# Optimization experiments

Hardware: AMD Instinct MI355X
Metric: run time of the kernel (lower is better)

The kernel has to match this reference:

```python
import jax, jax.numpy as jnp
import numpy as np

N, E, IN_F, H_F, OUT_F = 50000, 800000, 128, 128, 3
BN_EPS = 1e-5


def setup_inputs() -> dict:
    key = jax.random.key(0)
    ks = jax.random.split(key, 8)
    x = jax.random.normal(ks[0], (N, IN_F), dtype=jnp.float32)
    edge_index = jax.random.randint(ks[1], (2, E), 0, N, dtype=jnp.int64)
    edge_weight = jax.random.uniform(ks[2], (E,), dtype=jnp.float32)
    # GCNConv weight (Glorot-style scale) and bias
    conv_w = jax.random.normal(ks[3], (IN_F, H_F), dtype=jnp.float32) * (1.0 / np.sqrt(IN_F))
    conv_b = jnp.zeros((H_F,), dtype=jnp.float32)
    # BatchNorm affine params
    gamma = jnp.ones((H_F,), dtype=jnp.float32)
    beta = jnp.zeros((H_F,), dtype=jnp.float32)
    # Final linear
    lin_w = jax.random.normal(ks[4], (H_F, OUT_F), dtype=jnp.float32) * (1.0 / np.sqrt(H_F))
    lin_b = jnp.zeros((OUT_F,), dtype=jnp.float32)
    return {"x": x, "edge_index": edge_index, "edge_weight": edge_weight,
            "conv_w": conv_w, "conv_b": conv_b, "gamma": gamma, "beta": beta,
            "lin_w": lin_w, "lin_b": lin_b}


def _gcn_conv(x, edge_index, edge_weight, conv_w, conv_b):
    n = x.shape[0]
    # add self-loops with weight 1 (PyG GCNConv default)
    loops = jnp.arange(n, dtype=edge_index.dtype)
    row = jnp.concatenate([edge_index[0], loops])
    col = jnp.concatenate([edge_index[1], loops])
    ew = jnp.concatenate([edge_weight, jnp.ones((n,), dtype=edge_weight.dtype)])
    # symmetric normalization: deg over destination nodes
    deg = jax.ops.segment_sum(ew, col, num_segments=n)
    dinv = jnp.where(deg > 0, jax.lax.rsqrt(deg), 0.0)
    norm = dinv[row] * ew * dinv[col]            # [E+N]
    h = x @ conv_w                                # [N, h_f]
    msg = h[row] * norm[:, None]                  # gather + scale, [E+N, h_f]
    agg = jax.ops.segment_sum(msg, col, num_segments=n)  # scatter-add
    return agg + conv_b


def reference(x, edge_index, edge_weight, conv_w, conv_b, gamma, beta, lin_w, lin_b):
    h = jax.nn.relu(_gcn_conv(x, edge_index, edge_weight, conv_w, conv_b))
    # BatchNorm1d over the node dimension (training-style batch stats, biased var)
    mean = jnp.mean(h, axis=0)
    var = jnp.mean((h - mean) ** 2, axis=0)
    hn = (h - mean) * jax.lax.rsqrt(var + BN_EPS) * gamma + beta
    # dropout is identity (deterministic eval-style reference)
    return hn @ lin_w + lin_b
```

## Files before the change

kernel.cpp:

```cpp
#include <hip/hip_runtime.h>

#define NN   50000
#define NE   800000
#define FH   128
#define NOUT 3
#define BN_EPS 1e-5f

#define CAP  48
#define EWS  65535.0f
#define IEWS (1.0f / 65535.0f)
#define FXS  8388608.0f

#define GEMM_BLKS   782
#define BUCKET_BLKS 782
#define GATHER_BLKS 2048
#define RED_BLKS    (GATHER_BLKS / 256)

#define WS_H2      0
#define WS_AGG2    3200000
#define WS_BUCKET  6400000
#define WS_PACKED  8800000
#define WS_DINV    8900000
#define WS_PARTIAL 8950000
#define WS_STAGE2  9474288
#define WS_PREP    9476336

typedef __attribute__((ext_vector_type(8))) short  short8;
typedef __attribute__((ext_vector_type(4))) float  f32x4;

__device__ __forceinline__ unsigned int pack_bf16(float a, float b) {
    unsigned int ua = __float_as_uint(a);
    unsigned int ub = __float_as_uint(b);
    ua += 0x7fffu + ((ua >> 16) & 1u);
    ub += 0x7fffu + ((ub >> 16) & 1u);
    return (ua >> 16) | (ub & 0xffff0000u);
}
__device__ __forceinline__ unsigned short bf16_1(float a) {
    unsigned int ua = __float_as_uint(a);
    ua += 0x7fffu + ((ua >> 16) & 1u);
    return (unsigned short)(ua >> 16);
}
__device__ __forceinline__ float bf16_lo(unsigned int u) {
    return __uint_as_float(u << 16);
}
__device__ __forceinline__ float bf16_hi(unsigned int u) {
    return __uint_as_float(u & 0xffff0000u);
}

__global__ __launch_bounds__(256) void k_bucket(const int* __restrict__ ei,
                                                const float* __restrict__ ew,
                                                unsigned long long* __restrict__ packed,
                                                unsigned int* __restrict__ bucket) {
    const int e0 = blockIdx.x * 1024 + threadIdx.x;
    int                col[4];
    unsigned int       ent[4];
    unsigned long long add[4];
    int                ok[4];
#pragma unroll
    for (int k = 0; k < 4; ++k) {
        int e = e0 + k * 256;
        ok[k] = (e < NE);
        int ee = ok[k] ? e : 0;
        int row = ei[ee];
        col[k] = ei[NE + ee];
        float wv = ew[ee];
        ent[k] = ((unsigned int)row << 16) | __float2uint_rn(wv * EWS);
        add[k] = (1ULL << 32) | (unsigned long long)__float2uint_rn(wv * FXS);
    }
    int slot[4];
#pragma unroll
    for (int k = 0; k < 4; ++k)
        slot[k] = ok[k] ? (int)(atomicAdd(&packed[col[k]], add[k]) >> 32) : 0;
#pragma unroll
    for (int k = 0; k < 4; ++k)
        if (ok[k]) bucket[(size_t)col[k] * CAP + slot[k]] = ent[k];
}

__global__ __launch_bounds__(256) void k_gemm(const float* __restrict__ x,
                                              const float* __restrict__ w,
                                              unsigned int* __restrict__ h2,
                                              const unsigned long long* __restrict__ packed,
                                              float* __restrict__ dinv) {
    __shared__ unsigned short swB[32 * 64 * 8];
    const int tid = threadIdx.x;

    {
        int gi = blockIdx.x * 256 + tid;
        if (gi < NN) {
            unsigned int lo = (unsigned int)(packed[gi] & 0xffffffffu);
            dinv[gi] = rsqrtf((float)lo * (1.0f / FXS) + 1.0f);
        }
    }

#pragma unroll
    for (int it = 0; it < 8; ++it) {
        int s  = tid + it * 256;
        int l  = s & 63;
        int fs = s >> 6;
        int kc = fs >> 3, t = fs & 7;
        int n  = (l & 15) + 16 * t;
        int k0 = kc * 32 + (l >> 4) * 8;
        unsigned short* dst = &swB[s * 8];
#pragma unroll
        for (int j = 0; j < 8; ++j)
            dst[j] = bf16_1(w[(size_t)(k0 + j) * FH + n]);
    }
    __syncthreads();

    const int wv = tid >> 6, l = tid & 63;
    const int m = l & 15, q = l >> 4;
    int node = blockIdx.x * 64 + wv * 16 + m;
    if (node >= NN) node = NN - 1;

    f32x4 acc[8];
#pragma unroll
    for (int t = 0; t < 8; ++t) acc[t] = (f32x4){0.f, 0.f, 0.f, 0.f};

#pragma unroll
    for (int kc = 0; kc < 4; ++kc) {
        const float* xr = x + (size_t)node * FH + kc * 32 + q * 8;
        float4 a0 = *(const float4*)xr;
        float4 a1 = *(const float4*)(xr + 4);
        union { short8 s8; uint4 u4; } af;
        af.u4.x = pack_bf16(a0.x, a0.y);  af.u4.y = pack_bf16(a0.z, a0.w);
        af.u4.z = pack_bf16(a1.x, a1.y);  af.u4.w = pack_bf16(a1.z, a1.w);
#pragma unroll
        for (int t = 0; t < 8; ++t) {
            union { short8 s8; uint4 u4; } bf;
            bf.u4 = *(const uint4*)&swB[((kc * 8 + t) * 64 + l) * 8];
            acc[t] = __builtin_amdgcn_mfma_f32_16x16x32_bf16(af.s8, bf.s8, acc[t], 0, 0, 0);
        }
    }

    __syncthreads();
    unsigned short* sc = swB;
#pragma unroll
    for (int t = 0; t < 8; ++t) {
#pragma unroll
        for (int r = 0; r < 4; ++r) {
            int ml = wv * 16 + q * 4 + r;
            int f  = t * 16 + m;
            sc[ml * FH + f] = bf16_1(acc[t][r]);
        }
    }
    __syncthreads();
    const uint4* s4 = (const uint4*)sc;
#pragma unroll
    for (int i = 0; i < 4; ++i) {
        int u  = tid + i * 256;
        int nl = u >> 4;
        int ng = blockIdx.x * 64 + nl;
        if (ng < NN)
            *((uint4*)h2 + (size_t)ng * 16 + (u & 15)) = s4[u];
    }
}

__global__ __launch_bounds__(256) void k_gather(const unsigned int* __restrict__ h2,
                                                const float* __restrict__ dinv,
                                                const unsigned int* __restrict__ bucket,
                                                const unsigned long long* __restrict__ packed,
                                                const float* __restrict__ conv_b,
                                                unsigned int* __restrict__ agg2,
                                                float* __restrict__ partial) {
    const int lane = threadIdx.x & 63;
    const int wv   = threadIdx.x >> 6;
    float2 bv = *(const float2*)(conv_b + lane * 2);

    float sa = 0.f, sb = 0.f, sa2 = 0.f, sb2 = 0.f;

    for (int n = blockIdx.x * 4 + wv; n < NN; n += GATHER_BLKS * 4) {
        float dvn = dinv[n];
        unsigned int hself = h2[(size_t)n * 64 + lane];
        float ax = bf16_lo(hself) * dvn;
        float ay = bf16_hi(hself) * dvn;

        const unsigned int* bkt = bucket + (size_t)n * CAP;
        int c = (int)(packed[n] >> 32);
        int j = 0;
        for (; j + 8 <= c; j += 8) {
            uint4 b0 = *(const uint4*)(bkt + j);
            uint4 b1 = *(const uint4*)(bkt + j + 4);
            unsigned int u[8] = {b0.x, b0.y, b0.z, b0.w, b1.x, b1.y, b1.z, b1.w};
            float t[8];
            unsigned int q[8];
#pragma unroll
            for (int r = 0; r < 8; ++r) {
                int s = u[r] >> 16;
                t[r] = dinv[s] * (float)(u[r] & 0xffffu) * IEWS;
                q[r] = h2[(size_t)s * 64 + lane];
            }
#pragma unroll
            for (int r = 0; r < 8; ++r) {
                ax = fmaf(bf16_lo(q[r]), t[r], ax);
                ay = fmaf(bf16_hi(q[r]), t[r], ay);
            }
        }
        if (j + 4 <= c) {
            uint4 b0 = *(const uint4*)(bkt + j);
            unsigned int u[4] = {b0.x, b0.y, b0.z, b0.w};
#pragma unroll
            for (int r = 0; r < 4; ++r) {
                int s = u[r] >> 16;
                float t = dinv[s] * (float)(u[r] & 0xffffu) * IEWS;
                unsigned int q = h2[(size_t)s * 64 + lane];
                ax = fmaf(bf16_lo(q), t, ax);
                ay = fmaf(bf16_hi(q), t, ay);
            }
            j += 4;
        }
        for (; j < c; ++j) {
            unsigned int u0 = bkt[j];
            int s0 = u0 >> 16;
            float t0 = dinv[s0] * (float)(u0 & 0xffffu) * IEWS;
            unsigned int q0 = h2[(size_t)s0 * 64 + lane];
            ax = fmaf(bf16_lo(q0), t0, ax);  ay = fmaf(bf16_hi(q0), t0, ay);
        }

        float ox = fmaxf(fmaf(dvn, ax, bv.x), 0.f);
        float oy = fmaxf(fmaf(dvn, ay, bv.y), 0.f);
        agg2[(size_t)n * 64 + lane] = pack_bf16(ox, oy);

        sa += ox;  sa2 = fmaf(ox, ox, sa2);
        sb += oy;  sb2 = fmaf(oy, oy, sb2);
    }

    __shared__ float red[256];
    float vals[4] = {sa, sb, sa2, sb2};
    float* pb = partial + (size_t)blockIdx.x * 256;
#pragma unroll
    for (int r = 0; r < 4; ++r) {
        red[threadIdx.x] = vals[r];
        __syncthreads();
        if (wv == 0) {
            float t = red[lane] + red[lane + 64] + red[lane + 128] + red[lane + 192];
            pb[((r < 2) ? 0 : FH) + 2 * lane + (r & 1)] = t;
        }
        __syncthreads();
    }
}

__global__ __launch_bounds__(256) void k_red(const float* __restrict__ partial,
                                             float* __restrict__ stage2) {
    int i = threadIdx.x;
    const float* base = partial + (size_t)blockIdx.x * 256 * 256;
    float acc = 0.f;
    for (int j = 0; j < 256; ++j) acc += base[j * 256 + i];
    stage2[blockIdx.x * 256 + i] = acc;
}

__global__ void k_prep(const float* __restrict__ stage2,
                       const float* __restrict__ gamma,
                       const float* __restrict__ beta,
                       const float* __restrict__ lin_w,
                       const float* __restrict__ lin_b,
                       float* __restrict__ prep) {
    __shared__ float ssum[256];
    __shared__ float red[3 * FH];
    int i = threadIdx.x;
    float acc = 0.f;
#pragma unroll
    for (int r = 0; r < RED_BLKS; ++r) acc += stage2[r * 256 + i];
    ssum[i] = acc;
    __syncthreads();
    if (i < FH) {
        float mean = ssum[i] * (1.0f / NN);
        float var  = ssum[FH + i] * (1.0f / NN) - mean * mean;
        float inv  = rsqrtf(var + BN_EPS);
        float sc   = inv * gamma[i];
        float sh   = fmaf(-mean, sc, beta[i]);
#pragma unroll
        for (int o = 0; o < NOUT; ++o) {
            float lw = lin_w[i * NOUT + o];
            prep[i * NOUT + o] = sc * lw;
            red[o * FH + i]    = sh * lw;
        }
    }
    __syncthreads();
    if (i < NOUT) {
        float s = lin_b[i];
        for (int f = 0; f < FH; ++f) s += red[i * FH + f];
        prep[3 * FH + i] = s;
    }
}

__global__ __launch_bounds__(256) void k_final(const unsigned int* __restrict__ agg2,
                                               const float* __restrict__ prep,
                                               float* __restrict__ out) {
    int n = blockIdx.x * 4 + (threadIdx.x >> 6);
    int lane = threadIdx.x & 63;
    int f0 = lane * 2, f1 = lane * 2 + 1;

    unsigned int v = agg2[(size_t)n * 64 + lane];
    float vx = bf16_lo(v), vy = bf16_hi(v);

    float o0 = vx * prep[f0 * NOUT + 0] + vy * prep[f1 * NOUT + 0];
    float o1 = vx * prep[f0 * NOUT + 1] + vy * prep[f1 * NOUT + 1];
    float o2 = vx * prep[f0 * NOUT + 2] + vy * prep[f1 * NOUT + 2];

#pragma unroll
    for (int off = 32; off > 0; off >>= 1) {
        o0 += __shfl_down(o0, off, 64);
        o1 += __shfl_down(o1, off, 64);
        o2 += __shfl_down(o2, off, 64);
    }
    if (lane == 0) {
        out[n * NOUT + 0] = o0 + prep[3 * FH + 0];
        out[n * NOUT + 1] = o1 + prep[3 * FH + 1];
        out[n * NOUT + 2] = o2 + prep[3 * FH + 2];
    }
}

extern "C" void kernel_launch(void* const* d_in, const int* in_sizes, int n_in,
                              void* d_out, int out_size, void* d_ws, size_t ws_size,
                              hipStream_t stream) {
    const float* x      = (const float*)d_in[0];
    const int*   ei     = (const int*)d_in[1];
    const float* ew     = (const float*)d_in[2];
    const float* conv_w = (const float*)d_in[3];
    const float* conv_b = (const float*)d_in[4];
    const float* gamma  = (const float*)d_in[5];
    const float* beta   = (const float*)d_in[6];
    const float* lin_w  = (const float*)d_in[7];
    const float* lin_b  = (const float*)d_in[8];
    float* out = (float*)d_out;
    float* ws  = (float*)d_ws;

    unsigned int*       h2      = (unsigned int*)(ws + WS_H2);
    unsigned int*       agg2    = (unsigned int*)(ws + WS_AGG2);
    unsigned int*       bucket  = (unsigned int*)(ws + WS_BUCKET);
    unsigned long long* packed  = (unsigned long long*)(ws + WS_PACKED);
    float*              dinv    = ws + WS_DINV;
    float*              partial = ws + WS_PARTIAL;
    float*              stage2  = ws + WS_STAGE2;
    float*              prep    = ws + WS_PREP;

    hipMemsetAsync(packed, 0, (size_t)NN * sizeof(unsigned long long), stream);

    k_bucket<<<BUCKET_BLKS, 256, 0, stream>>>(ei, ew, packed, bucket);
    k_gemm  <<<GEMM_BLKS,   256, 0, stream>>>(x, conv_w, h2, packed, dinv);
    k_gather<<<GATHER_BLKS, 256, 0, stream>>>(h2, dinv, bucket, packed, conv_b, agg2, partial);
    k_red   <<<RED_BLKS,    256, 0, stream>>>(partial, stage2);
    k_prep  <<<1,           256, 0, stream>>>(stage2, gamma, beta, lin_w, lin_b, prep);
    k_final <<<NN / 4,      256, 0, stream>>>(agg2, prep, out);
}
```

Baseline: 194.6 us.

## Fuse edge bucketing with GEMM kernel and compute dinv on the fly in gather

Merges the edge-bucketing kernel and the feature GEMM into one launch, with even blocks doing the GEMM and odd blocks doing the bucketing, so the two independent phases run concurrently and one launch disappears. The dinv array is dropped. The gather kernel recomputes rsqrt of the degree for each neighbor from the low word of the packed counter, which removes a separate write and read pass. The cost is an extra rsqrt per edge and 8-byte-strided reads of the packed array in the gather.

```diff
diff --git a/kernel.cpp b/kernel.cpp
--- a/kernel.cpp
+++ b/kernel.cpp
@@ -10,9 +10,9 @@
 #define EWS  65535.0f
 #define IEWS (1.0f / 65535.0f)
 #define FXS  8388608.0f
-
-#define GEMM_BLKS   782
-#define BUCKET_BLKS 782
+#define IFXS (1.0f / 8388608.0f)
+
+#define FUSED_BLKS  1564
 #define GATHER_BLKS 2048
 #define RED_BLKS    (GATHER_BLKS / 256)
 
@@ -20,10 +20,9 @@
 #define WS_AGG2    3200000
 #define WS_BUCKET  6400000
 #define WS_PACKED  8800000
-#define WS_DINV    8900000
-#define WS_PARTIAL 8950000
-#define WS_STAGE2  9474288
-#define WS_PREP    9476336
+#define WS_PARTIAL 8900000
+#define WS_STAGE2  9424288
+#define WS_PREP    9426336
 
 typedef __attribute__((ext_vector_type(8))) short  short8;
 typedef __attribute__((ext_vector_type(4))) float  f32x4;
@@ -47,118 +46,110 @@
     return __uint_as_float(u & 0xffff0000u);
 }
 
-__global__ __launch_bounds__(256) void k_bucket(const int* __restrict__ ei,
-                                                const float* __restrict__ ew,
-                                                unsigned long long* __restrict__ packed,
-                                                unsigned int* __restrict__ bucket) {
-    const int e0 = blockIdx.x * 1024 + threadIdx.x;
-    int                col[4];
-    unsigned int       ent[4];
-    unsigned long long add[4];
-    int                ok[4];
-#pragma unroll
-    for (int k = 0; k < 4; ++k) {
-        int e = e0 + k * 256;
-        ok[k] = (e < NE);
-        int ee = ok[k] ? e : 0;
-        int row = ei[ee];
-        col[k] = ei[NE + ee];
-        float wv = ew[ee];
-        ent[k] = ((unsigned int)row << 16) | __float2uint_rn(wv * EWS);
-        add[k] = (1ULL << 32) | (unsigned long long)__float2uint_rn(wv * FXS);
-    }
-    int slot[4];
-#pragma unroll
-    for (int k = 0; k < 4; ++k)
-        slot[k] = ok[k] ? (int)(atomicAdd(&packed[col[k]], add[k]) >> 32) : 0;
-#pragma unroll
-    for (int k = 0; k < 4; ++k)
-        if (ok[k]) bucket[(size_t)col[k] * CAP + slot[k]] = ent[k];
-}
-
-__global__ __launch_bounds__(256) void k_gemm(const float* __restrict__ x,
-                                              const float* __restrict__ w,
-                                              unsigned int* __restrict__ h2,
-                                              const unsigned long long* __restrict__ packed,
-                                              float* __restrict__ dinv) {
+__global__ __launch_bounds__(256) void k_gemm_bucket(
+        const float* __restrict__ x, const float* __restrict__ w,
+        unsigned int* __restrict__ h2,
+        const int* __restrict__ ei, const float* __restrict__ ew,
+        unsigned long long* __restrict__ packed,
+        unsigned int* __restrict__ bucket) {
     __shared__ unsigned short swB[32 * 64 * 8];
     const int tid = threadIdx.x;
 
-    {
-        int gi = blockIdx.x * 256 + tid;
-        if (gi < NN) {
-            unsigned int lo = (unsigned int)(packed[gi] & 0xffffffffu);
-            dinv[gi] = rsqrtf((float)lo * (1.0f / FXS) + 1.0f);
-        }
-    }
-
-#pragma unroll
-    for (int it = 0; it < 8; ++it) {
-        int s  = tid + it * 256;
-        int l  = s & 63;
-        int fs = s >> 6;
-        int kc = fs >> 3, t = fs & 7;
-        int n  = (l & 15) + 16 * t;
-        int k0 = kc * 32 + (l >> 4) * 8;
-        unsigned short* dst = &swB[s * 8];
-#pragma unroll
-        for (int j = 0; j < 8; ++j)
-            dst[j] = bf16_1(w[(size_t)(k0 + j) * FH + n]);
-    }
-    __syncthreads();
-
-    const int wv = tid >> 6, l = tid & 63;
-    const int m = l & 15, q = l >> 4;
-    int node = blockIdx.x * 64 + wv * 16 + m;
-    if (node >= NN) node = NN - 1;
-
-    f32x4 acc[8];
-#pragma unroll
-    for (int t = 0; t < 8; ++t) acc[t] = (f32x4){0.f, 0.f, 0.f, 0.f};
-
-#pragma unroll
-    for (int kc = 0; kc < 4; ++kc) {
-        const float* xr = x + (size_t)node * FH + kc * 32 + q * 8;
-        float4 a0 = *(const float4*)xr;
-        float4 a1 = *(const float4*)(xr + 4);
-        union { short8 s8; uint4 u4; } af;
-        af.u4.x = pack_bf16(a0.x, a0.y);  af.u4.y = pack_bf16(a0.z, a0.w);
-        af.u4.z = pack_bf16(a1.x, a1.y);  af.u4.w = pack_bf16(a1.z, a1.w);
+    if ((blockIdx.x & 1) == 0) {
+        const int gblk = blockIdx.x >> 1;
+#pragma unroll
+        for (int it = 0; it < 8; ++it) {
+            int s  = tid + it * 256;
+            int l  = s & 63;
+            int fs = s >> 6;
+            int kc = fs >> 3, t = fs & 7;
+            int n  = (l & 15) + 16 * t;
+            int k0 = kc * 32 + (l >> 4) * 8;
+            unsigned short* dst = &swB[s * 8];
+#pragma unroll
+            for (int j = 0; j < 8; ++j)
+                dst[j] = bf16_1(w[(size_t)(k0 + j) * FH + n]);
+        }
+        __syncthreads();
+
+        const int wv = tid >> 6, l = tid & 63;
+        const int m = l & 15, q = l >> 4;
+        int node = gblk * 64 + wv * 16 + m;
+        if (node >= NN) node = NN - 1;
+
+        f32x4 acc[8];
+#pragma unroll
+        for (int t = 0; t < 8; ++t) acc[t] = (f32x4){0.f, 0.f, 0.f, 0.f};
+
+#pragma unroll
+        for (int kc = 0; kc < 4; ++kc) {
+            const float* xr = x + (size_t)node * FH + kc * 32 + q * 8;
+            float4 a0 = *(const float4*)xr;
+            float4 a1 = *(const float4*)(xr + 4);
+            union { short8 s8; uint4 u4; } af;
+            af.u4.x = pack_bf16(a0.x, a0.y);  af.u4.y = pack_bf16(a0.z, a0.w);
+            af.u4.z = pack_bf16(a1.x, a1.y);  af.u4.w = pack_bf16(a1.z, a1.w);
+#pragma unroll
+            for (int t = 0; t < 8; ++t) {
+                union { short8 s8; uint4 u4; } bf;
+                bf.u4 = *(const uint4*)&swB[((kc * 8 + t) * 64 + l) * 8];
+                acc[t] = __builtin_amdgcn_mfma_f32_16x16x32_bf16(af.s8, bf.s8, acc[t], 0, 0, 0);
+            }
+        }
+
+        __syncthreads();
+        unsigned short* sc = swB;
 #pragma unroll
         for (int t = 0; t < 8; ++t) {
-            union { short8 s8; uint4 u4; } bf;
-            bf.u4 = *(const uint4*)&swB[((kc * 8 + t) * 64 + l) * 8];
-            acc[t] = __builtin_amdgcn_mfma_f32_16x16x32_bf16(af.s8, bf.s8, acc[t], 0, 0, 0);
-        }
-    }
-
-    __syncthreads();
-    unsigned short* sc = swB;
-#pragma unroll
-    for (int t = 0; t < 8; ++t) {
-#pragma unroll
-        for (int r = 0; r < 4; ++r) {
-            int ml = wv * 16 + q * 4 + r;
-            int f  = t * 16 + m;
-            sc[ml * FH + f] = bf16_1(acc[t][r]);
-        }
-    }
-    __syncthreads();
-    const uint4* s4 = (const uint4*)sc;
-#pragma unroll
-    for (int i = 0; i < 4; ++i) {
-        int u  = tid + i * 256;
-        int nl = u >> 4;
-        int ng = blockIdx.x * 64 + nl;
-        if (ng < NN)
-            *((uint4*)h2 + (size_t)ng * 16 + (u & 15)) = s4[u];
+#pragma unroll
+            for (int r = 0; r < 4; ++r) {
+                int ml = wv * 16 + q * 4 + r;
+                int f  = t * 16 + m;
+                sc[ml * FH + f] = bf16_1(acc[t][r]);
+            }
+        }
+        __syncthreads();
+        const uint4* s4 = (const uint4*)sc;
+#pragma unroll
+        for (int i = 0; i < 4; ++i) {
+            int u  = tid + i * 256;
+            int nl = u >> 4;
+            int ng = gblk * 64 + nl;
+            if (ng < NN)
+                *((uint4*)h2 + (size_t)ng * 16 + (u & 15)) = s4[u];
+        }
+    } else {
+        const int bidx = blockIdx.x >> 1;
+        const int e0 = bidx * 1024 + tid;
+        int                col[4];
+        unsigned int       ent[4];
+        unsigned long long add[4];
+        int                ok[4];
+#pragma unroll
+        for (int k = 0; k < 4; ++k) {
+            int e = e0 + k * 256;
+            ok[k] = (e < NE);
+            int ee = ok[k] ? e : 0;
+            int row = ei[ee];
+            col[k] = ei[NE + ee];
+            float wv2 = ew[ee];
+            ent[k] = ((unsigned int)row << 16) | __float2uint_rn(wv2 * EWS);
+            add[k] = (1ULL << 32) | (unsigned long long)__float2uint_rn(wv2 * FXS);
+        }
+        int slot[4];
+#pragma unroll
+        for (int k = 0; k < 4; ++k)
+            slot[k] = ok[k] ? (int)(atomicAdd(&packed[col[k]], add[k]) >> 32) : 0;
+#pragma unroll
+        for (int k = 0; k < 4; ++k)
+            if (ok[k]) bucket[(size_t)col[k] * CAP + slot[k]] = ent[k];
     }
 }
 
 __global__ __launch_bounds__(256) void k_gather(const unsigned int* __restrict__ h2,
-                                                const float* __restrict__ dinv,
+                                                const unsigned int* __restrict__ packedlo,
+                                                const unsigned long long* __restrict__ packed,
                                                 const unsigned int* __restrict__ bucket,
-                                                const unsigned long long* __restrict__ packed,
                                                 const float* __restrict__ conv_b,
                                                 unsigned int* __restrict__ agg2,
                                                 float* __restrict__ partial) {
@@ -169,13 +160,15 @@
     float sa = 0.f, sb = 0.f, sa2 = 0.f, sb2 = 0.f;
 
     for (int n = blockIdx.x * 4 + wv; n < NN; n += GATHER_BLKS * 4) {
-        float dvn = dinv[n];
+        unsigned long long pk = packed[n];
+        int c = (int)(pk >> 32);
+        float dvn = rsqrtf((float)(unsigned int)(pk & 0xffffffffu) * IFXS + 1.0f);
+
         unsigned int hself = h2[(size_t)n * 64 + lane];
         float ax = bf16_lo(hself) * dvn;
         float ay = bf16_hi(hself) * dvn;
 
         const unsigned int* bkt = bucket + (size_t)n * CAP;
-        int c = (int)(packed[n] >> 32);
         int j = 0;
         for (; j + 8 <= c; j += 8) {
             uint4 b0 = *(const uint4*)(bkt + j);
@@ -186,7 +179,8 @@
 #pragma unroll
             for (int r = 0; r < 8; ++r) {
                 int s = u[r] >> 16;
-                t[r] = dinv[s] * (float)(u[r] & 0xffffu) * IEWS;
+                float ds = rsqrtf((float)packedlo[2 * s] * IFXS + 1.0f);
+                t[r] = ds * (float)(u[r] & 0xffffu) * IEWS;
                 q[r] = h2[(size_t)s * 64 + lane];
             }
 #pragma unroll
@@ -201,7 +195,8 @@
 #pragma unroll
             for (int r = 0; r < 4; ++r) {
                 int s = u[r] >> 16;
-                float t = dinv[s] * (float)(u[r] & 0xffffu) * IEWS;
+                float ds = rsqrtf((float)packedlo[2 * s] * IFXS + 1.0f);
+                float t = ds * (float)(u[r] & 0xffffu) * IEWS;
                 unsigned int q = h2[(size_t)s * 64 + lane];
                 ax = fmaf(bf16_lo(q), t, ax);
                 ay = fmaf(bf16_hi(q), t, ay);
@@ -211,7 +206,8 @@
         for (; j < c; ++j) {
             unsigned int u0 = bkt[j];
             int s0 = u0 >> 16;
-            float t0 = dinv[s0] * (float)(u0 & 0xffffu) * IEWS;
+            float ds = rsqrtf((float)packedlo[2 * s0] * IFXS + 1.0f);
+            float t0 = ds * (float)(u0 & 0xffffu) * IEWS;
             unsigned int q0 = h2[(size_t)s0 * 64 + lane];
             ax = fmaf(bf16_lo(q0), t0, ax);  ay = fmaf(bf16_hi(q0), t0, ay);
         }
@@ -329,16 +325,15 @@
     unsigned int*       agg2    = (unsigned int*)(ws + WS_AGG2);
     unsigned int*       bucket  = (unsigned int*)(ws + WS_BUCKET);
     unsigned long long* packed  = (unsigned long long*)(ws + WS_PACKED);
-    float*              dinv    = ws + WS_DINV;
     float*              partial = ws + WS_PARTIAL;
     float*              stage2  = ws + WS_STAGE2;
     float*              prep    = ws + WS_PREP;
 
     hipMemsetAsync(packed, 0, (size_t)NN * sizeof(unsigned long long), stream);
 
-    k_bucket<<<BUCKET_BLKS, 256, 0, stream>>>(ei, ew, packed, bucket);
-    k_gemm  <<<GEMM_BLKS,   256, 0, stream>>>(x, conv_w, h2, packed, dinv);
-    k_gather<<<GATHER_BLKS, 256, 0, stream>>>(h2, dinv, bucket, packed, conv_b, agg2, partial);
+    k_gemm_bucket<<<FUSED_BLKS, 256, 0, stream>>>(x, conv_w, h2, ei, ew, packed, bucket);
+    k_gather<<<GATHER_BLKS, 256, 0, stream>>>(h2, (const unsigned int*)packed, packed,
+                                              bucket, conv_b, agg2, partial);
     k_red   <<<RED_BLKS,    256, 0, stream>>>(partial, stage2);
     k_prep  <<<1,           256, 0, stream>>>(stage2, gamma, beta, lin_w, lin_b, prep);
     k_final <<<NN / 4,      256, 0, stream>>>(agg2, prep, out);
```

Result: slower. 201.2 us (+3.4%).
